# Optimization experiments

Hardware: AMD Instinct MI355X
Metric: run time of the kernel (lower is better)

The kernel has to match this reference:

```python
import jax, jax.numpy as jnp
import numpy as np

B = 131072
USER_N = 100000
ITEM_N = 20000
CONCEPT_N = 128
D_IN = 3
NB_MOD_MAX = 12
M = NB_MOD_MAX + 2  # nb_mod_max_plus_sent


def setup_inputs() -> dict:
    key = jax.random.key(0)
    ks = jax.random.split(key, 7)
    user_ids = jax.random.randint(ks[0], (B,), 0, USER_N)
    item_ids = jax.random.randint(ks[1], (B,), 0, ITEM_N)
    concept_ids = jax.random.randint(ks[2], (B,), 0, CONCEPT_N)
    users_emb_weight = jax.random.normal(ks[3], (USER_N, CONCEPT_N), dtype=jnp.float32)
    item_resp_weight = jax.random.normal(ks[4], (ITEM_N * M, D_IN), dtype=jnp.float32)
    W = jax.random.normal(ks[5], (CONCEPT_N, D_IN, CONCEPT_N), dtype=jnp.float32)
    # nb_modalities in [2, nb_mod_max]; mask[i, j] = 0 for j in [1, nb_modalities[i]], inf elsewhere
    nb_modalities = jax.random.randint(ks[6], (ITEM_N,), 2, NB_MOD_MAX + 1)
    cols = jnp.arange(M)[None, :]  # (1, M)
    valid = (cols >= 1) & (cols <= nb_modalities[:, None])
    mask = jnp.where(valid, 0.0, jnp.inf).astype(jnp.float32)  # (ITEM_N, M)
    return {
        "user_ids": user_ids,
        "item_ids": item_ids,
        "concept_ids": concept_ids,
        "users_emb_weight": users_emb_weight,
        "item_resp_weight": item_resp_weight,
        "W": W,
        "mask": mask,
        "nb_modalities": nb_modalities,
    }


def reference(user_ids, item_ids, concept_ids, users_emb_weight, item_resp_weight, W, mask, nb_modalities):
    # W_t: (B, d_in, C)
    W_t = W[concept_ids]
    # im_idx: (B, M) row indices into the item-response embedding table
    im_idx = item_ids[:, None] * M + jnp.arange(M)[None, :]
    im_emb_prime = item_resp_weight[im_idx]  # (B, M, d_in)
    # bmm: (B, M, d_in) x (B, d_in, C) -> (B, M, C)
    im_emb = jnp.einsum('bmd,bdc->bmc', im_emb_prime, W_t)
    u_emb = users_emb_weight[user_ids]  # (B, C)
    diff = u_emb[:, None, :] - im_emb
    p_uim = jnp.sum(diff * diff, axis=2)  # (B, M)
    idx = jnp.argmin(p_uim + mask[item_ids, :], axis=1)  # (B,)
    nb = nb_modalities[item_ids]
    # mod_to_resp: ((idx - 1) / (nb - 1)) + 1
    responses = (idx.astype(jnp.float32) - 1.0) / (nb.astype(jnp.float32) - 1.0) + 1.0
    return responses
```

## Files before the change

kernel.cpp:

```cpp
#include <hip/hip_runtime.h>
#include <math.h>

static constexpr int B_TOTAL = 131072;
static constexpr int M_MOD   = 14;
static constexpr int C_DIM   = 128;

template <int CTRL>
__device__ __forceinline__ float dpp_mov(float x) {
    return __int_as_float(__builtin_amdgcn_update_dpp(
        0, __float_as_int(x), CTRL, 0xF, 0xF, true));
}
#define ROW_SUM(x)                                                             \
    do {                                                                       \
        x += dpp_mov<0x128>(x);                                 \
        x += dpp_mov<0x124>(x);                                 \
        x += dpp_mov<0x04E>(x);                \
        x += dpp_mov<0x0B1>(x);                \
    } while (0)
#define ROW_MIN(x)                                                             \
    do {                                                                       \
        x = fminf(x, dpp_mov<0x128>(x));                                       \
        x = fminf(x, dpp_mov<0x124>(x));                                       \
        x = fminf(x, dpp_mov<0x04E>(x));                                       \
        x = fminf(x, dpp_mov<0x0B1>(x));                                       \
    } while (0)

__global__ __launch_bounds__(64) void gram_kernel(
    const float* __restrict__ W, float* __restrict__ g)
{
    const int c = blockIdx.x;
    const int l = threadIdx.x;
    const float2* wp = (const float2*)(W + (size_t)c * 3 * C_DIM);
    const float2 a0 = wp[l], a1 = wp[64 + l], a2 = wp[128 + l];
    float g00 = a0.x * a0.x + a0.y * a0.y;
    float g01 = a0.x * a1.x + a0.y * a1.y;
    float g02 = a0.x * a2.x + a0.y * a2.y;
    float g11 = a1.x * a1.x + a1.y * a1.y;
    float g12 = a1.x * a2.x + a1.y * a2.y;
    float g22 = a2.x * a2.x + a2.y * a2.y;
#pragma unroll
    for (int off = 32; off; off >>= 1) {
        g00 += __shfl_xor(g00, off, 64);
        g01 += __shfl_xor(g01, off, 64);
        g02 += __shfl_xor(g02, off, 64);
        g11 += __shfl_xor(g11, off, 64);
        g12 += __shfl_xor(g12, off, 64);
        g22 += __shfl_xor(g22, off, 64);
    }
    if (l == 0) {
        float* o = g + c * 8;
        o[0] = g00; o[1] = g01; o[2] = g02;
        o[3] = g11; o[4] = g12; o[5] = g22;
        o[6] = 0.f; o[7] = 0.f;
    }
}

__global__ __launch_bounds__(256) void impact_kernel(
    const int*   __restrict__ user_ids,
    const int*   __restrict__ item_ids,
    const int*   __restrict__ concept_ids,
    const float* __restrict__ users_emb,
    const float* __restrict__ item_resp,
    const float* __restrict__ W,
    const int*   __restrict__ nb_mod,
    const float* __restrict__ gram,
    float*       __restrict__ out)
{
    const int s = threadIdx.x & 15;
    const int b = blockIdx.x * 16 + (threadIdx.x >> 4);

    const int uid = user_ids[b];
    const int iid = item_ids[b];
    const int cid = concept_ids[b];
    const int nb  = nb_mod[iid];

    const float4* up = (const float4*)(users_emb + (size_t)uid * C_DIM);
    const float4 uA = up[s], uB = up[s + 16];
    const float4* wp = (const float4*)(W + (size_t)cid * 3 * C_DIM);
    const float4 w0a = wp[s],      w0b = wp[16 + s];
    const float4 w1a = wp[32 + s], w1b = wp[48 + s];
    const float4 w2a = wp[64 + s], w2b = wp[80 + s];
    const float4 gA = ((const float4*)(gram + cid * 8))[0];
    const float4 gB = ((const float4*)(gram + cid * 8))[1];
    const float* pj = item_resp + ((size_t)iid * M_MOD + (s < 12 ? s + 1 : 1)) * 3;
    const float p0 = pj[0], p1 = pj[1], p2 = pj[2];

    float v0 = 0.f, v1 = 0.f, v2 = 0.f;
#define COL(uc, a0, a1, a2)                                                    \
    do {                                                                       \
        v0 = fmaf((a0), (uc), v0);                                             \
        v1 = fmaf((a1), (uc), v1);                                             \
        v2 = fmaf((a2), (uc), v2);                                             \
    } while (0)
    COL(uA.x, w0a.x, w1a.x, w2a.x);
    COL(uA.y, w0a.y, w1a.y, w2a.y);
    COL(uA.z, w0a.z, w1a.z, w2a.z);
    COL(uA.w, w0a.w, w1a.w, w2a.w);
    COL(uB.x, w0b.x, w1b.x, w2b.x);
    COL(uB.y, w0b.y, w1b.y, w2b.y);
    COL(uB.z, w0b.z, w1b.z, w2b.z);
    COL(uB.w, w0b.w, w1b.w, w2b.w);
#undef COL
    ROW_SUM(v0);
    ROW_SUM(v1);
    ROW_SUM(v2);

    float m = INFINITY;
    if (s < 12 && (s + 1) <= nb) {
        const float dot = fmaf(p0, v0, fmaf(p1, v1, p2 * v2));
        float q = p0 * p0 * gA.x;
        q = fmaf(p1 * p1, gA.w, q);
        q = fmaf(p2 * p2, gB.y, q);
        q = fmaf(2.0f * p0 * p1, gA.y, q);
        q = fmaf(2.0f * p0 * p2, gA.z, q);
        q = fmaf(2.0f * p1 * p2, gB.x, q);
        m = fmaf(-2.0f, dot, q);
    }
    float bm = m;
    ROW_MIN(bm);
    const unsigned long long mask = __ballot(m == bm);
    if (s == 0) {
        const int group = (threadIdx.x >> 4) & 3;
        const unsigned slice = (unsigned)((mask >> (group * 16)) & 0xffffu);
        const int jm1 = __builtin_ctz(slice);
        out[b] = (float)jm1 / (float)(nb - 1) + 1.0f;
    }
}

extern "C" void kernel_launch(void* const* d_in, const int* in_sizes, int n_in,
                              void* d_out, int out_size, void* d_ws, size_t ws_size,
                              hipStream_t stream) {
    const int*   user_ids    = (const int*)d_in[0];
    const int*   item_ids    = (const int*)d_in[1];
    const int*   concept_ids = (const int*)d_in[2];
    const float* users_emb   = (const float*)d_in[3];
    const float* item_resp   = (const float*)d_in[4];
    const float* W           = (const float*)d_in[5];
    const int*   nb_mod      = (const int*)d_in[7];
    float*       gram        = (float*)d_ws;
    float*       out         = (float*)d_out;

    gram_kernel<<<dim3(128), dim3(64), 0, stream>>>(W, gram);
    impact_kernel<<<dim3(B_TOTAL / 16), dim3(256), 0, stream>>>(
        user_ids, item_ids, concept_ids, users_emb, item_resp, W, nb_mod,
        gram, out);
}
```

Measured before the change: 113.7 us.

## Process eight batch rows per group with software-pipelined prefetch of ids and user rows

Each 16-lane group now handles eight batch entries in an unrolled loop instead of one. The ids are fetched two iterations ahead and the user embedding row one iteration ahead, using double-buffered registers so gather latency overlaps compute. The grid shrinks eightfold and launch bounds request four blocks per CU. The cost is higher register pressure and fewer waves available to hide latency through occupancy.

```diff
diff --git a/kernel.cpp b/kernel.cpp
--- a/kernel.cpp
+++ b/kernel.cpp
@@ -4,6 +4,7 @@
 static constexpr int B_TOTAL = 131072;
 static constexpr int M_MOD   = 14;
 static constexpr int C_DIM   = 128;
+static constexpr int CPB     = 8;
 
 template <int CTRL>
 __device__ __forceinline__ float dpp_mov(float x) {
@@ -55,7 +56,7 @@
     }
 }
 
-__global__ __launch_bounds__(256) void impact_kernel(
+__global__ __launch_bounds__(256, 4) void impact_kernel(
     const int*   __restrict__ user_ids,
     const int*   __restrict__ item_ids,
     const int*   __restrict__ concept_ids,
@@ -66,64 +67,90 @@
     const float* __restrict__ gram,
     float*       __restrict__ out)
 {
-    const int s = threadIdx.x & 15;
-    const int b = blockIdx.x * 16 + (threadIdx.x >> 4);
+    const int s    = threadIdx.x & 15;
+    const int g    = threadIdx.x >> 4;
+    const int base = blockIdx.x * (CPB * 16) + g;
 
-    const int uid = user_ids[b];
-    const int iid = item_ids[b];
-    const int cid = concept_ids[b];
-    const int nb  = nb_mod[iid];
+    int uid[CPB], iid[CPB], cid[CPB];
+    float4 uA[2], uB[2];
 
-    const float4* up = (const float4*)(users_emb + (size_t)uid * C_DIM);
-    const float4 uA = up[s], uB = up[s + 16];
-    const float4* wp = (const float4*)(W + (size_t)cid * 3 * C_DIM);
-    const float4 w0a = wp[s],      w0b = wp[16 + s];
-    const float4 w1a = wp[32 + s], w1b = wp[48 + s];
-    const float4 w2a = wp[64 + s], w2b = wp[80 + s];
-    const float4 gA = ((const float4*)(gram + cid * 8))[0];
-    const float4 gB = ((const float4*)(gram + cid * 8))[1];
-    const float* pj = item_resp + ((size_t)iid * M_MOD + (s < 12 ? s + 1 : 1)) * 3;
-    const float p0 = pj[0], p1 = pj[1], p2 = pj[2];
+    uid[0] = user_ids[base];      iid[0] = item_ids[base];
+    cid[0] = concept_ids[base];
+    uid[1] = user_ids[base + 16]; iid[1] = item_ids[base + 16];
+    cid[1] = concept_ids[base + 16];
+    {
+        const float4* up = (const float4*)(users_emb + (size_t)uid[0] * C_DIM);
+        uA[0] = up[s]; uB[0] = up[s + 16];
+    }
 
-    float v0 = 0.f, v1 = 0.f, v2 = 0.f;
+#pragma unroll
+    for (int t = 0; t < CPB; ++t) {
+        if (t + 2 < CPB) {
+            const int bn = base + (t + 2) * 16;
+            uid[t + 2] = user_ids[bn];
+            iid[t + 2] = item_ids[bn];
+            cid[t + 2] = concept_ids[bn];
+        }
+        if (t + 1 < CPB) {
+            const float4* up =
+                (const float4*)(users_emb + (size_t)uid[t + 1] * C_DIM);
+            uA[(t + 1) & 1] = up[s];
+            uB[(t + 1) & 1] = up[s + 16];
+        }
+
+        const int I  = iid[t];
+        const int Cc = cid[t];
+        const int nb = nb_mod[I];
+        const float4* wp = (const float4*)(W + (size_t)Cc * 3 * C_DIM);
+        const float4 w0a = wp[s],      w0b = wp[16 + s];
+        const float4 w1a = wp[32 + s], w1b = wp[48 + s];
+        const float4 w2a = wp[64 + s], w2b = wp[80 + s];
+        const float4 gA = ((const float4*)(gram + Cc * 8))[0];
+        const float4 gB = ((const float4*)(gram + Cc * 8))[1];
+        const float* pj =
+            item_resp + ((size_t)I * M_MOD + (s < 12 ? s + 1 : 1)) * 3;
+        const float p0 = pj[0], p1 = pj[1], p2 = pj[2];
+
+        const float4 uAc = uA[t & 1], uBc = uB[t & 1];
+        float v0 = 0.f, v1 = 0.f, v2 = 0.f;
 #define COL(uc, a0, a1, a2)                                                    \
-    do {                                                                       \
-        v0 = fmaf((a0), (uc), v0);                                             \
-        v1 = fmaf((a1), (uc), v1);                                             \
-        v2 = fmaf((a2), (uc), v2);                                             \
-    } while (0)
-    COL(uA.x, w0a.x, w1a.x, w2a.x);
-    COL(uA.y, w0a.y, w1a.y, w2a.y);
-    COL(uA.z, w0a.z, w1a.z, w2a.z);
-    COL(uA.w, w0a.w, w1a.w, w2a.w);
-    COL(uB.x, w0b.x, w1b.x, w2b.x);
-    COL(uB.y, w0b.y, w1b.y, w2b.y);
-    COL(uB.z, w0b.z, w1b.z, w2b.z);
-    COL(uB.w, w0b.w, w1b.w, w2b.w);
+        do {                                                                   \
+            v0 = fmaf((a0), (uc), v0);                                         \
+            v1 = fmaf((a1), (uc), v1);                                         \
+            v2 = fmaf((a2), (uc), v2);                                         \
+        } while (0)
+        COL(uAc.x, w0a.x, w1a.x, w2a.x);
+        COL(uAc.y, w0a.y, w1a.y, w2a.y);
+        COL(uAc.z, w0a.z, w1a.z, w2a.z);
+        COL(uAc.w, w0a.w, w1a.w, w2a.w);
+        COL(uBc.x, w0b.x, w1b.x, w2b.x);
+        COL(uBc.y, w0b.y, w1b.y, w2b.y);
+        COL(uBc.z, w0b.z, w1b.z, w2b.z);
+        COL(uBc.w, w0b.w, w1b.w, w2b.w);
 #undef COL
-    ROW_SUM(v0);
-    ROW_SUM(v1);
-    ROW_SUM(v2);
+        ROW_SUM(v0);
+        ROW_SUM(v1);
+        ROW_SUM(v2);
 
-    float m = INFINITY;
-    if (s < 12 && (s + 1) <= nb) {
-        const float dot = fmaf(p0, v0, fmaf(p1, v1, p2 * v2));
-        float q = p0 * p0 * gA.x;
-        q = fmaf(p1 * p1, gA.w, q);
-        q = fmaf(p2 * p2, gB.y, q);
-        q = fmaf(2.0f * p0 * p1, gA.y, q);
-        q = fmaf(2.0f * p0 * p2, gA.z, q);
-        q = fmaf(2.0f * p1 * p2, gB.x, q);
-        m = fmaf(-2.0f, dot, q);
-    }
-    float bm = m;
-    ROW_MIN(bm);
-    const unsigned long long mask = __ballot(m == bm);
-    if (s == 0) {
-        const int group = (threadIdx.x >> 4) & 3;
-        const unsigned slice = (unsigned)((mask >> (group * 16)) & 0xffffu);
-        const int jm1 = __builtin_ctz(slice);
-        out[b] = (float)jm1 / (float)(nb - 1) + 1.0f;
+        float m = INFINITY;
+        if (s < 12 && (s + 1) <= nb) {
+            const float dot = fmaf(p0, v0, fmaf(p1, v1, p2 * v2));
+            float q = p0 * p0 * gA.x;
+            q = fmaf(p1 * p1, gA.w, q);
+            q = fmaf(p2 * p2, gB.y, q);
+            q = fmaf(2.0f * p0 * p1, gA.y, q);
+            q = fmaf(2.0f * p0 * p2, gA.z, q);
+            q = fmaf(2.0f * p1 * p2, gB.x, q);
+            m = fmaf(-2.0f, dot, q);
+        }
+        float bm = m;
+        ROW_MIN(bm);
+        const unsigned long long mask = __ballot(m == bm);
+        if (s == 0) {
+            const unsigned slice = (unsigned)((mask >> ((g & 3) * 16)) & 0xffffu);
+            const int jm1 = __builtin_ctz(slice);
+            out[base + t * 16] = (float)jm1 / (float)(nb - 1) + 1.0f;
+        }
     }
 }
 
@@ -141,7 +168,7 @@
     float*       out         = (float*)d_out;
 
     gram_kernel<<<dim3(128), dim3(64), 0, stream>>>(W, gram);
-    impact_kernel<<<dim3(B_TOTAL / 16), dim3(256), 0, stream>>>(
+    impact_kernel<<<dim3(B_TOTAL / (CPB * 16)), dim3(256), 0, stream>>>(
         user_ids, item_ids, concept_ids, users_emb, item_resp, W, nb_mod,
         gram, out);
 }
```

After: 114.2 us. No clear change (+0.4%).
